# Kernel optimization log

Measured on AMD Instinct MI355X. Metric: run time of the kernel, lower is better.

Reference implementation:

```python
import jax, jax.numpy as jnp
import numpy as np

EMBED_DIM = 1024
NUM_HEADS = 16
HEAD_DIM = EMBED_DIM // NUM_HEADS


def setup_inputs() -> dict:
    key = jax.random.key(0)
    kx, kq, kk, kv, kbq, kbk, kbv = jax.random.split(key, 7)
    s = 1.0 / np.sqrt(EMBED_DIM)
    return {
        "x": jax.random.normal(kx, (4, 2048, EMBED_DIM), dtype=jnp.float32),
        "Wq": jax.random.uniform(kq, (EMBED_DIM, EMBED_DIM), jnp.float32, -s, s),
        "bq": jax.random.uniform(kbq, (EMBED_DIM,), jnp.float32, -s, s),
        "Wk": jax.random.uniform(kk, (EMBED_DIM, EMBED_DIM), jnp.float32, -s, s),
        "bk": jax.random.uniform(kbk, (EMBED_DIM,), jnp.float32, -s, s),
        "Wv": jax.random.uniform(kv, (EMBED_DIM, EMBED_DIM), jnp.float32, -s, s),
        "bv": jax.random.uniform(kbv, (EMBED_DIM,), jnp.float32, -s, s),
    }


def reference(x, Wq, bq, Wk, bk, Wv, bv):
    B, S, E = x.shape
    H, D = NUM_HEADS, HEAD_DIM
    # QKV projections; reshape to (B, H, S, D)
    def proj(W, b):
        return (x @ W + b).reshape(B, S, H, D).transpose(0, 2, 1, 3)
    Q = proj(Wq, bq)
    K = proj(Wk, bk)
    V = proj(Wv, bv)
    scale = jnp.asarray(np.sqrt(D), x.dtype)
    scores = jnp.einsum("bhqd,bhkd->bhqk", Q, K) / scale
    attn = jax.nn.softmax(scores, axis=-1)
    out = jnp.einsum("bhqk,bhkd->bhqd", attn, V)
    return out.transpose(0, 2, 1, 3).reshape(B, S, E)
```

## Files before the change

### kernel.cpp

```cpp
#include <hip/hip_runtime.h>
#include <math.h>

typedef unsigned short u16;
typedef __bf16 bf16x8 __attribute__((ext_vector_type(8)));
typedef float f32x4 __attribute__((ext_vector_type(4)));
typedef u16 u16x8 __attribute__((ext_vector_type(8)));
typedef u16 u16x4 __attribute__((ext_vector_type(4)));
typedef short s16x4 __attribute__((ext_vector_type(4)));
typedef unsigned u32x2 __attribute__((ext_vector_type(2)));
typedef unsigned u32x4 __attribute__((ext_vector_type(4)));

#define BB 4
#define SS 2048
#define EE 1024
#define HH 16
#define DH 64
#define PLANE (SS * DH)

__device__ __forceinline__ u16 f32_to_bf16(float f) {
  unsigned u = __builtin_bit_cast(unsigned, f);
  u += 0x7fffu + ((u >> 16) & 1u);
  return (u16)(u >> 16);
}

__device__ __forceinline__ unsigned pack_bf16_trunc(float lo, float hi) {
  return __builtin_amdgcn_perm(__builtin_bit_cast(unsigned, hi),
                               __builtin_bit_cast(unsigned, lo), 0x07060302u);
}

__device__ __forceinline__ void async_copy16(const void* g, void* lds) {
  __builtin_amdgcn_global_load_lds(
      (const __attribute__((address_space(1))) void*)g,
      (__attribute__((address_space(3))) void*)lds, 16, 0, 0);
}

__device__ __forceinline__ float ex2(float x) {
#if __has_builtin(__builtin_amdgcn_exp2f)
  return __builtin_amdgcn_exp2f(x);
#else
  float r;
  asm("v_exp_f32 %0, %1\n\ts_nop 1" : "=v"(r) : "v"(x));
  return r;
#endif
}

__global__ void cvt_x_kernel(const float* __restrict__ x, u16* __restrict__ xb) {
  int i = (blockIdx.x * 256 + threadIdx.x) * 8;
  float4 a = *(const float4*)(x + i);
  float4 c = *(const float4*)(x + i + 4);
  u16x8 o;
  o[0] = f32_to_bf16(a.x); o[1] = f32_to_bf16(a.y);
  o[2] = f32_to_bf16(a.z); o[3] = f32_to_bf16(a.w);
  o[4] = f32_to_bf16(c.x); o[5] = f32_to_bf16(c.y);
  o[6] = f32_to_bf16(c.z); o[7] = f32_to_bf16(c.w);
  *(u16x8*)(xb + i) = o;
}

__global__ void cvt_w_kernel(const float* __restrict__ Wq, const float* __restrict__ Wk,
                             const float* __restrict__ Wv, u16* __restrict__ wb) {
  __shared__ u16 T[64 * 72];
  int mat = blockIdx.z;
  const float* W = (mat == 0) ? Wq : ((mat == 1) ? Wk : Wv);
  int e0 = blockIdx.x * 64, k0 = blockIdx.y * 64;
  int t = threadIdx.x;
  int tr = t >> 4, tc = t & 15;
  for (int i = 0; i < 4; ++i) {
    int k = i * 16 + tr;
    float4 v = *(const float4*)(W + (k0 + k) * EE + e0 + tc * 4);
    T[(tc * 4 + 0) * 72 + k] = f32_to_bf16(v.x);
    T[(tc * 4 + 1) * 72 + k] = f32_to_bf16(v.y);
    T[(tc * 4 + 2) * 72 + k] = f32_to_bf16(v.z);
    T[(tc * 4 + 3) * 72 + k] = f32_to_bf16(v.w);
  }
  __syncthreads();
  u16* out = wb + (size_t)(mat * EE + e0) * EE + k0;
  for (int i = 0; i < 4; ++i) {
    int e = i * 16 + tr;
    u16x4 v = *(u16x4*)&T[e * 72 + tc * 4];
    *(u16x4*)(out + e * EE + tc * 4) = v;
  }
}

__global__ __launch_bounds__(256) void qkv_gemm_kernel(
    const u16* __restrict__ A, const u16* __restrict__ Bt,
    const float* __restrict__ bq, const float* __restrict__ bk,
    const float* __restrict__ bv, u16* __restrict__ qkv) {
  __shared__ u16 As0[128 * 64], Bs0[128 * 64];
  __shared__ u16 As1[128 * 64], Bs1[128 * 64];
  int tid = threadIdx.x;
  int lane = tid & 63, w = tid >> 6;
  int ln = lane & 15, quad = lane >> 4;
  int wm = w & 1, wn = w >> 1;
  int bn = blockIdx.x, bm = blockIdx.y;
  const u16* Ag = A + (size_t)bm * 128 * EE;
  const u16* Bg = Bt + (size_t)bn * 128 * EE;

  int r8 = lane >> 3, c8 = lane & 7;
  int sc8 = (c8 ^ r8) * 8;

  f32x4 acc[4][4] = {};

  auto STAGE = [&](u16* AsD, u16* BsD, int kt) {
    int k0 = kt * 64;
#pragma unroll
    for (int i = 0; i < 4; ++i) {
      int row0 = i * 32 + w * 8;
      async_copy16(Ag + (row0 + r8) * EE + k0 + sc8, AsD + (i * 256 + w * 64) * 8);
      async_copy16(Bg + (row0 + r8) * EE + k0 + sc8, BsD + (i * 256 + w * 64) * 8);
    }
  };

  int k7 = ln & 7;
  int ks0 = (quad ^ k7) * 8;
  int ks1 = ks0 ^ 32;

  auto TILE = [&](const u16* AsB, const u16* BsB) {
    __builtin_amdgcn_s_setprio(1);
    bf16x8 b0[4], b1[4];
#pragma unroll
    for (int ni = 0; ni < 4; ++ni) {
      const u16* br = BsB + (wn * 64 + ni * 16 + ln) * 64;
      b0[ni] = *(const bf16x8*)(br + ks0);
      b1[ni] = *(const bf16x8*)(br + ks1);
    }
#pragma unroll
    for (int mi = 0; mi < 4; ++mi) {
      const u16* ar = AsB + (wm * 64 + mi * 16 + ln) * 64;
      bf16x8 a0 = *(const bf16x8*)(ar + ks0);
      bf16x8 a1 = *(const bf16x8*)(ar + ks1);
#pragma unroll
      for (int ni = 0; ni < 4; ++ni) {
        acc[mi][ni] = __builtin_amdgcn_mfma_f32_16x16x32_bf16(a0, b0[ni],
                                                              acc[mi][ni], 0, 0, 0);
        acc[mi][ni] = __builtin_amdgcn_mfma_f32_16x16x32_bf16(a1, b1[ni],
                                                              acc[mi][ni], 0, 0, 0);
      }
    }
    __builtin_amdgcn_s_setprio(0);
  };

  STAGE(As0, Bs0, 0);
#pragma unroll 1
  for (int kt = 0; kt < 16; kt += 2) {
    STAGE(As1, Bs1, kt + 1);
    asm volatile("s_waitcnt vmcnt(8)" ::: "memory");
    __builtin_amdgcn_sched_barrier(0);
    __builtin_amdgcn_s_barrier();
    __builtin_amdgcn_sched_barrier(0);
    TILE(As0, Bs0);
    __builtin_amdgcn_s_barrier();
    if (kt + 2 < 16) {
      STAGE(As0, Bs0, kt + 2);
      asm volatile("s_waitcnt vmcnt(8)" ::: "memory");
    } else {
      asm volatile("s_waitcnt vmcnt(0)" ::: "memory");
    }
    __builtin_amdgcn_sched_barrier(0);
    __builtin_amdgcn_s_barrier();
    __builtin_amdgcn_sched_barrier(0);
    TILE(As1, Bs1);
    __builtin_amdgcn_s_barrier();
  }

  int mat = bn >> 3;
  const float* bias = (mat == 0) ? bq : ((mat == 1) ? bk : bv);
  int b = bm >> 4;
  if (mat < 2) {
    float scl = (mat == 0) ? 0.18033688011112042f : 1.0f;
    int base0 = (mat * BB + b) * HH * PLANE;
    for (int ni = 0; ni < 4; ++ni) {
      int e = (bn & 7) * 128 + wn * 64 + ni * 16 + ln;
      float bve = bias[e];
      int hh = e >> 6, d = e & 63;
      int cb = base0 + hh * PLANE + d;
      for (int mi = 0; mi < 4; ++mi) {
        int s0 = (bm & 15) * 128 + wm * 64 + mi * 16 + quad * 4;
        for (int r = 0; r < 4; ++r)
          qkv[cb + (s0 + r) * DH] = f32_to_bf16((acc[mi][ni][r] + bve) * scl);
      }
    }
  } else {
    size_t base0 = (size_t)(2 * BB + b) * HH * PLANE;
    for (int ni = 0; ni < 4; ++ni) {
      int e = (bn & 7) * 128 + wn * 64 + ni * 16 + ln;
      float bve = bias[e];
      int hh = e >> 6, d = e & 63;
      size_t cb = base0 + (size_t)hh * PLANE + (size_t)d * SS;
      for (int mi = 0; mi < 4; ++mi) {
        int s0 = (bm & 15) * 128 + wm * 64 + mi * 16 + quad * 4;
        u16x4 vv;
        for (int r = 0; r < 4; ++r) vv[r] = f32_to_bf16(acc[mi][ni][r] + bve);
        *(u16x4*)(qkv + cb + s0) = vv;
      }
    }
  }
}

__global__ __launch_bounds__(256, 4) void attn_kernel(const u16* __restrict__ qkv,
                                                      float* __restrict__ out) {
  __shared__ u16 Ks0[64 * 64], Ks1[64 * 64];
  __shared__ u16 Vs0[64 * 64], Vs1[64 * 64];
  int wg = blockIdx.x + (blockIdx.y << 4) + (blockIdx.z << 8);
  int xcd = wg & 7, idx = wg >> 3;
  int bh = xcd * 8 + (idx >> 4);
  int qb = idx & 15;
  int h = bh & 15, b = bh >> 4;
  int t = threadIdx.x;
  int lane = t & 63, w = t >> 6;
  int ln = lane & 15, quad = lane >> 4;
  int k7 = ln & 7;
  int q0 = quad & 1, q1 = quad >> 1;
  const u16* Qg = qkv + (size_t)bh * PLANE + qb * 128 * DH;
  const u16* Kg = qkv + (size_t)(BB * HH + bh) * PLANE;
  const u16* Vg = qkv + (size_t)(2 * BB * HH + bh) * PLANE;

  int r8 = lane >> 3, c8 = lane & 7;
  int sc8 = (c8 ^ r8) * 8;

  auto STAGE = [&](u16* KsD, u16* VsD, int kt) {
    const u16* Kt = Kg + kt * 64 * DH;
    const u16* Vt = Vg + kt * 64;
#pragma unroll
    for (int i = 0; i < 2; ++i) {
      int row = w * 16 + i * 8 + r8;
      async_copy16(Kt + row * DH + sc8, KsD + (w * 16 + i * 8) * DH);
      async_copy16(Vt + row * SS + sc8, VsD + (w * 16 + i * 8) * DH);
    }
  };

  bf16x8 bq[2][2];
#pragma unroll
  for (int rb = 0; rb < 2; ++rb)
#pragma unroll
    for (int s = 0; s < 2; ++s)
      bq[rb][s] = *(const bf16x8*)(Qg + (w * 32 + rb * 16 + ln) * DH + s * 32 + quad * 8);

  u32x4 ow;
  ow[0] = ow[1] = ow[2] = ow[3] = 0x3F803F80u;
  bf16x8 ones8 = __builtin_bit_cast(bf16x8, ow);

  const f32x4 kz = {};
  f32x4 o[4][2] = {};
  f32x4 lacc[2] = {};

  int ks0 = (quad ^ k7) * 8;
  int ks1 = ks0 ^ 32;

  auto TILE = [&](const u16* Ksb, const u16* Vsb) {
    __builtin_amdgcn_s_setprio(1);
    f32x4 s[2][4];
#pragma unroll
    for (int g = 0; g < 4; ++g) {
      const u16* krow = Ksb + (g * 16 + ln) * DH;
      bf16x8 kf0 = *(const bf16x8*)(krow + ks0);
      bf16x8 kf1 = *(const bf16x8*)(krow + ks1);
      s[0][g] = __builtin_amdgcn_mfma_f32_16x16x32_bf16(kf0, bq[0][0], kz, 0, 0, 0);
      s[0][g] = __builtin_amdgcn_mfma_f32_16x16x32_bf16(kf1, bq[0][1], s[0][g], 0, 0, 0);
      s[1][g] = __builtin_amdgcn_mfma_f32_16x16x32_bf16(kf0, bq[1][0], kz, 0, 0, 0);
      s[1][g] = __builtin_amdgcn_mfma_f32_16x16x32_bf16(kf1, bq[1][1], s[1][g], 0, 0, 0);
    }
    bf16x8 af[2][2];
#pragma unroll
    for (int rb = 0; rb < 2; ++rb) {
      unsigned Wd[4][2];
#pragma unroll
      for (int g = 0; g < 4; ++g) {
        Wd[g][0] = pack_bf16_trunc(ex2(s[rb][g][0]), ex2(s[rb][g][1]));
        Wd[g][1] = pack_bf16_trunc(ex2(s[rb][g][2]), ex2(s[rb][g][3]));
      }
#pragma unroll
      for (int G = 0; G < 2; ++G) {
        u32x4 aw;
        aw[0] = Wd[2 * G][0];     aw[1] = Wd[2 * G][1];
        aw[2] = Wd[2 * G + 1][0]; aw[3] = Wd[2 * G + 1][1];
        af[rb][G] = __builtin_bit_cast(bf16x8, aw);
      }
      lacc[rb] = __builtin_amdgcn_mfma_f32_16x16x32_bf16(af[rb][0], ones8, lacc[rb], 0, 0, 0);
      lacc[rb] = __builtin_amdgcn_mfma_f32_16x16x32_bf16(af[rb][1], ones8, lacc[rb], 0, 0, 0);
    }
#pragma unroll
    for (int G = 0; G < 2; ++G) {
      int uLo = ((4 * G + q1) ^ k7) * 8 + 4 * q0;
      int uHi = ((4 * G + q1 + 2) ^ k7) * 8 + 4 * q0;
#pragma unroll
      for (int dg = 0; dg < 4; ++dg) {
        const u16* vrow = Vsb + (dg * 16 + ln) * DH;
        u32x2 lo = *(const u32x2*)(vrow + uLo);
        u32x2 hi = *(const u32x2*)(vrow + uHi);
        u32x4 vv;
        vv[0] = lo[0]; vv[1] = lo[1]; vv[2] = hi[0]; vv[3] = hi[1];
        bf16x8 vf = __builtin_bit_cast(bf16x8, vv);
        o[dg][0] = __builtin_amdgcn_mfma_f32_16x16x32_bf16(af[0][G], vf, o[dg][0], 0, 0, 0);
        o[dg][1] = __builtin_amdgcn_mfma_f32_16x16x32_bf16(af[1][G], vf, o[dg][1], 0, 0, 0);
      }
    }
    __builtin_amdgcn_s_setprio(0);
  };

  STAGE(Ks0, Vs0, 0);
#pragma unroll 1
  for (int kt = 0; kt < 32; kt += 2) {
    STAGE(Ks1, Vs1, kt + 1);
    asm volatile("s_waitcnt vmcnt(4)" ::: "memory");
    __builtin_amdgcn_sched_barrier(0);
    __builtin_amdgcn_s_barrier();
    __builtin_amdgcn_sched_barrier(0);
    TILE(Ks0, Vs0);
    __builtin_amdgcn_s_barrier();
    if (kt + 2 < 32) {
      STAGE(Ks0, Vs0, kt + 2);
      asm volatile("s_waitcnt vmcnt(4)" ::: "memory");
    } else {
      asm volatile("s_waitcnt vmcnt(0)" ::: "memory");
    }
    __builtin_amdgcn_sched_barrier(0);
    __builtin_amdgcn_s_barrier();
    __builtin_amdgcn_sched_barrier(0);
    TILE(Ks1, Vs1);
    __builtin_amdgcn_s_barrier();
  }

  int sb = qb * 128 + w * 32;
  float* og = out + (size_t)b * SS * EE + (size_t)h * DH;
#pragma unroll
  for (int rb = 0; rb < 2; ++rb)
#pragma unroll
    for (int r = 0; r < 4; ++r) {
      float ir = 1.0f / lacc[rb][r];
      size_t qrow = (size_t)(sb + rb * 16 + quad * 4 + r);
#pragma unroll
      for (int dg = 0; dg < 4; ++dg)
        og[qrow * EE + dg * 16 + ln] = o[dg][rb][r] * ir;
    }
}

extern "C" void kernel_launch(void* const* d_in, const int* in_sizes, int n_in,
                              void* d_out, int out_size, void* d_ws, size_t ws_size,
                              hipStream_t stream) {
  (void)in_sizes; (void)n_in; (void)out_size; (void)ws_size;
  const float* x  = (const float*)d_in[0];
  const float* Wq = (const float*)d_in[1];
  const float* bq = (const float*)d_in[2];
  const float* Wk = (const float*)d_in[3];
  const float* bk = (const float*)d_in[4];
  const float* Wv = (const float*)d_in[5];
  const float* bv = (const float*)d_in[6];
  float* out = (float*)d_out;

  u16* xb  = (u16*)d_out;
  u16* wb  = xb + (size_t)BB * SS * EE;
  u16* qkv = (u16*)d_ws;

  cvt_x_kernel<<<dim3((BB * SS * EE) / (256 * 8)), 256, 0, stream>>>(x, xb);
  cvt_w_kernel<<<dim3(16, 16, 3), 256, 0, stream>>>(Wq, Wk, Wv, wb);
  qkv_gemm_kernel<<<dim3(24, 64), 256, 0, stream>>>(xb, wb, bq, bk, bv, qkv);
  attn_kernel<<<dim3(SS / 128, HH, BB), 256, 0, stream>>>(qkv, out);
}
```

Measured before the change: 244.7 us.

## Double attention query tile to 256 rows per block and merge conversion kernels

The attention kernel now runs 512 threads (8 waves) per block, each block covering 256 query rows, so every K/V tile staged in LDS is reused by twice as many waves and the grid halves to 512 blocks. Each wave now issues one async copy per matrix per stage, so the vmcnt waits are lowered to match. Separately, the x and W fp32-to-bf16 conversion kernels are merged into one launch to save a kernel launch. The risks are fewer blocks for load balancing across CUs, larger barrier groups, and possible register pressure from the 512-thread launch bound.

```diff
diff --git a/kernel.cpp b/kernel.cpp
--- a/kernel.cpp
+++ b/kernel.cpp
@@ -44,25 +44,29 @@
 #endif
 }
 
-__global__ void cvt_x_kernel(const float* __restrict__ x, u16* __restrict__ xb) {
-  int i = (blockIdx.x * 256 + threadIdx.x) * 8;
-  float4 a = *(const float4*)(x + i);
-  float4 c = *(const float4*)(x + i + 4);
-  u16x8 o;
-  o[0] = f32_to_bf16(a.x); o[1] = f32_to_bf16(a.y);
-  o[2] = f32_to_bf16(a.z); o[3] = f32_to_bf16(a.w);
-  o[4] = f32_to_bf16(c.x); o[5] = f32_to_bf16(c.y);
-  o[6] = f32_to_bf16(c.z); o[7] = f32_to_bf16(c.w);
-  *(u16x8*)(xb + i) = o;
-}
-
-__global__ void cvt_w_kernel(const float* __restrict__ Wq, const float* __restrict__ Wk,
-                             const float* __restrict__ Wv, u16* __restrict__ wb) {
+__global__ __launch_bounds__(256) void cvt_kernel(
+    const float* __restrict__ x, const float* __restrict__ Wq,
+    const float* __restrict__ Wk, const float* __restrict__ Wv,
+    u16* __restrict__ xb, u16* __restrict__ wb) {
   __shared__ u16 T[64 * 72];
-  int mat = blockIdx.z;
+  int bid = blockIdx.x;
+  int t = threadIdx.x;
+  if (bid < 4096) {
+    int i = (bid * 256 + t) * 8;
+    float4 a = *(const float4*)(x + i);
+    float4 c = *(const float4*)(x + i + 4);
+    u16x8 o;
+    o[0] = f32_to_bf16(a.x); o[1] = f32_to_bf16(a.y);
+    o[2] = f32_to_bf16(a.z); o[3] = f32_to_bf16(a.w);
+    o[4] = f32_to_bf16(c.x); o[5] = f32_to_bf16(c.y);
+    o[6] = f32_to_bf16(c.z); o[7] = f32_to_bf16(c.w);
+    *(u16x8*)(xb + i) = o;
+    return;
+  }
+  int wid = bid - 4096;
+  int mat = wid >> 8, r = wid & 255;
   const float* W = (mat == 0) ? Wq : ((mat == 1) ? Wk : Wv);
-  int e0 = blockIdx.x * 64, k0 = blockIdx.y * 64;
-  int t = threadIdx.x;
+  int e0 = (r & 15) * 64, k0 = (r >> 4) * 64;
   int tr = t >> 4, tc = t & 15;
   for (int i = 0; i < 4; ++i) {
     int k = i * 16 + tr;
@@ -196,21 +200,21 @@
   }
 }
 
-__global__ __launch_bounds__(256, 4) void attn_kernel(const u16* __restrict__ qkv,
+__global__ __launch_bounds__(512, 4) void attn_kernel(const u16* __restrict__ qkv,
                                                       float* __restrict__ out) {
   __shared__ u16 Ks0[64 * 64], Ks1[64 * 64];
   __shared__ u16 Vs0[64 * 64], Vs1[64 * 64];
-  int wg = blockIdx.x + (blockIdx.y << 4) + (blockIdx.z << 8);
+  int wg = blockIdx.x;
   int xcd = wg & 7, idx = wg >> 3;
-  int bh = xcd * 8 + (idx >> 4);
-  int qb = idx & 15;
+  int bh = xcd * 8 + (idx >> 3);
+  int qb = idx & 7;
   int h = bh & 15, b = bh >> 4;
   int t = threadIdx.x;
   int lane = t & 63, w = t >> 6;
   int ln = lane & 15, quad = lane >> 4;
   int k7 = ln & 7;
   int q0 = quad & 1, q1 = quad >> 1;
-  const u16* Qg = qkv + (size_t)bh * PLANE + qb * 128 * DH;
+  const u16* Qg = qkv + (size_t)bh * PLANE + qb * 256 * DH;
   const u16* Kg = qkv + (size_t)(BB * HH + bh) * PLANE;
   const u16* Vg = qkv + (size_t)(2 * BB * HH + bh) * PLANE;
 
@@ -220,12 +224,9 @@
   auto STAGE = [&](u16* KsD, u16* VsD, int kt) {
     const u16* Kt = Kg + kt * 64 * DH;
     const u16* Vt = Vg + kt * 64;
-#pragma unroll
-    for (int i = 0; i < 2; ++i) {
-      int row = w * 16 + i * 8 + r8;
-      async_copy16(Kt + row * DH + sc8, KsD + (w * 16 + i * 8) * DH);
-      async_copy16(Vt + row * SS + sc8, VsD + (w * 16 + i * 8) * DH);
-    }
+    int row = w * 8 + r8;
+    async_copy16(Kt + row * DH + sc8, KsD + (w * 8) * DH);
+    async_copy16(Vt + row * SS + sc8, VsD + (w * 8) * DH);
   };
 
   bf16x8 bq[2][2];
@@ -301,7 +302,7 @@
 #pragma unroll 1
   for (int kt = 0; kt < 32; kt += 2) {
     STAGE(Ks1, Vs1, kt + 1);
-    asm volatile("s_waitcnt vmcnt(4)" ::: "memory");
+    asm volatile("s_waitcnt vmcnt(2)" ::: "memory");
     __builtin_amdgcn_sched_barrier(0);
     __builtin_amdgcn_s_barrier();
     __builtin_amdgcn_sched_barrier(0);
@@ -309,7 +310,7 @@
     __builtin_amdgcn_s_barrier();
     if (kt + 2 < 32) {
       STAGE(Ks0, Vs0, kt + 2);
-      asm volatile("s_waitcnt vmcnt(4)" ::: "memory");
+      asm volatile("s_waitcnt vmcnt(2)" ::: "memory");
     } else {
       asm volatile("s_waitcnt vmcnt(0)" ::: "memory");
     }
@@ -320,7 +321,7 @@
     __builtin_amdgcn_s_barrier();
   }
 
-  int sb = qb * 128 + w * 32;
+  int sb = qb * 256 + w * 32;
   float* og = out + (size_t)b * SS * EE + (size_t)h * DH;
 #pragma unroll
   for (int rb = 0; rb < 2; ++rb)
@@ -351,8 +352,7 @@
   u16* wb  = xb + (size_t)BB * SS * EE;
   u16* qkv = (u16*)d_ws;
 
-  cvt_x_kernel<<<dim3((BB * SS * EE) / (256 * 8)), 256, 0, stream>>>(x, xb);
-  cvt_w_kernel<<<dim3(16, 16, 3), 256, 0, stream>>>(Wq, Wk, Wv, wb);
+  cvt_kernel<<<dim3(4096 + 768), 256, 0, stream>>>(x, Wq, Wk, Wv, xb, wb);
   qkv_gemm_kernel<<<dim3(24, 64), 256, 0, stream>>>(xb, wb, bq, bk, bv, qkv);
-  attn_kernel<<<dim3(SS / 128, HH, BB), 256, 0, stream>>>(qkv, out);
-}
+  attn_kernel<<<dim3(512), 512, 0, stream>>>(qkv, out);
+}
```

Measured after the change: 226.8 us. 1.08x faster.
